# Optimization experiments

Hardware: AMD Instinct MI355X
Metric: run time of the kernel (lower is better)

## Reference

```python
import jax, jax.numpy as jnp
import numpy as np

C = 1000
D = 64
B = 2048
EPS_STATS = 1e-5   # eps in classwise_mean_cov
EPS_PREC = 1e-6    # clamp_min eps in _precision_from_covariance


def setup_inputs() -> dict:
    key = jax.random.key(0)
    kz, ky = jax.random.split(key)
    z = jax.random.normal(kz, (B, D), dtype=jnp.float32)
    y = jax.random.randint(ky, (B,), 0, C, dtype=jnp.int64)
    return {"z": z, "y": y}


def reference(z, y):
    # --- classwise_mean_cov (diag_covariance=True), via segment reductions ---
    # counts per class (+eps), same as one-hot column sums
    ones = jnp.ones((z.shape[0],), dtype=z.dtype)
    class_counts = jax.ops.segment_sum(ones, y, num_segments=C) + EPS_STATS  # (C,)
    class_prior = class_counts / class_counts.sum()                          # (C,)
    class_sums = jax.ops.segment_sum(z, y, num_segments=C)                   # (C,D)
    class_mean = class_sums / class_counts[:, None]                          # (C,D)
    # per-class variance: sum_b [y_b==c] (z_b - mu_c)^2 / counts_c
    centered = z - class_mean[y]                                             # (B,D)
    class_var = jax.ops.segment_sum(centered * centered, y, num_segments=C) / class_counts[:, None]
    pooled_cov = (class_prior[:, None] * class_var).sum(axis=0) + EPS_STATS  # (D,)

    # --- precision (diag): 1 / clamp_min(cov, eps) ---
    precision = 1.0 / jnp.maximum(pooled_cov, EPS_PREC)                      # (D,)

    # --- Mahalanobis scores over all classes ---
    diff = z[:, None, :] - class_mean[None, :, :]                            # (B,C,D)
    m2 = jnp.einsum('bcd,d,bcd->bc', diff, precision, diff)                  # (B,C)
    return jnp.log(class_prior)[None, :] - 0.5 * m2
```

## Files before the change

kernel.cpp:

```cpp
#include <hip/hip_runtime.h>
#include <hip/hip_bf16.h>
#include <math.h>

#define BB 2048
#define CC 1000
#define DD 64
#define NCB 125
#define NTB 16
constexpr float EPS_STATS = 1e-5f;
constexpr float EPS_PREC  = 1e-6f;
constexpr float TSUM = (float)BB + (float)CC * EPS_STATS;

typedef __attribute__((ext_vector_type(8))) short bf8;
typedef __attribute__((ext_vector_type(4))) float f32x4;

__device__ inline unsigned short f2bf(float f) {
    __hip_bfloat16 h = __float2bfloat16(f);
    return *reinterpret_cast<unsigned short*>(&h);
}

__global__ void __launch_bounds__(256)
k_stats(const float* __restrict__ z, const int* __restrict__ y,
        float* __restrict__ mean, float* __restrict__ logpr,
        float* __restrict__ corrPart, float* __restrict__ T2part) {
    int tid = threadIdx.x, bid = blockIdx.x;
    if (bid < NCB) {
        __shared__ __align__(16) int ys[BB];
        __shared__ int mlist[BB];
        __shared__ float sacc[8 * DD];
        __shared__ float corrv[8 * DD];
        __shared__ int cnts[8];
        __shared__ int mcnt;

        const int4* y4 = reinterpret_cast<const int4*>(y);
        int4* ys4 = reinterpret_cast<int4*>(ys);
        ys4[tid] = y4[tid];
        ys4[tid + 256] = y4[tid + 256];
        sacc[tid] = 0.f; sacc[tid + 256] = 0.f;
        if (tid < 8) cnts[tid] = 0;
        if (tid == 0) mcnt = 0;
        __syncthreads();

        int cbase = bid * 8;
        #pragma unroll
        for (int i = 0; i < BB / 256; ++i) {
            int b = tid + i * 256;
            int cl = ys[b] - cbase;
            if ((unsigned)cl < 8u) {
                atomicAdd(&cnts[cl], 1);
                int p = atomicAdd(&mcnt, 1);
                mlist[p] = b * 8 + cl;
            }
        }
        __syncthreads();

        int n = mcnt;
        int w = tid >> 6, lane = tid & 63;
        int eg = w * 4 + (lane >> 4);
        int d4 = (lane & 15) * 4;
        for (int j0 = 0; j0 < n; j0 += 16) {
            int j = j0 + eg;
            if (j < n) {
                int e = mlist[j];
                float4 v = *reinterpret_cast<const float4*>(
                    &z[(size_t)(e >> 3) * DD + d4]);
                float* sa = &sacc[(e & 7) * DD + d4];
                atomicAdd(sa + 0, v.x);
                atomicAdd(sa + 1, v.y);
                atomicAdd(sa + 2, v.z);
                atomicAdd(sa + 3, v.w);
            }
        }
        __syncthreads();

        #pragma unroll
        for (int i = 0; i < 2; ++i) {
            int idx = tid + i * 256;
            int cl = idx >> 6, d = idx & 63;
            float s  = sacc[idx];
            float nn = (float)cnts[cl];
            float ce = nn + EPS_STATS;
            float inv = 1.0f / ce;
            int c = cbase + cl;
            mean[(size_t)c * DD + d] = s * inv;
            if (d == 0) logpr[c] = logf(ce / TSUM);
            corrv[idx] = s * s * (nn + 2.f * EPS_STATS) * inv * inv;
        }
        __syncthreads();
        if (tid < DD) {
            float a = 0.f;
            #pragma unroll
            for (int cl = 0; cl < 8; ++cl) a += corrv[cl * DD + tid];
            corrPart[bid * DD + tid] = a;
        }
    } else {
        __shared__ float p2[4][DD];
        int tb = bid - NCB;
        int d = tid & 63, grp = tid >> 6;
        int r0 = tb * 128 + grp * 32;
        float a = 0.f;
        #pragma unroll 8
        for (int r = 0; r < 32; ++r) {
            float v = z[(size_t)(r0 + r) * DD + d];
            a = fmaf(v, v, a);
        }
        p2[grp][d] = a;
        __syncthreads();
        if (tid < DD)
            T2part[tb * DD + tid] =
                p2[0][tid] + p2[1][tid] + p2[2][tid] + p2[3][tid];
    }
}

__global__ void __launch_bounds__(256)
k_score_mfma(const float* __restrict__ z, const float* __restrict__ mean,
             const float* __restrict__ logpr, const float* __restrict__ corrPart,
             const float* __restrict__ T2part, float* __restrict__ out) {
    __shared__ __align__(16) float red[16][DD];
    __shared__ float ps_s[DD];
    int tid = threadIdx.x;

    {
        int r0 = tid >> 4;
        int c4 = (tid & 15) * 4;
        float4 t = *reinterpret_cast<const float4*>(&T2part[r0 * DD + c4]);
        float ax = t.x, ay = t.y, az = t.z, aw = t.w;
        for (int p = r0; p < NCB; p += 16) {
            float4 v = *reinterpret_cast<const float4*>(&corrPart[p * DD + c4]);
            ax -= v.x; ay -= v.y; az -= v.z; aw -= v.w;
        }
        float4 a4 = {ax, ay, az, aw};
        *reinterpret_cast<float4*>(&red[r0][c4]) = a4;
    }
    __syncthreads();
    if (tid < DD) {
        float acc = 0.f;
        #pragma unroll
        for (int g = 0; g < 16; ++g) acc += red[g][tid];
        float pooled = acc / TSUM + EPS_STATS;
        ps_s[tid] = 1.0f / fmaxf(pooled, EPS_PREC);
    }
    __syncthreads();

    int wv = tid >> 6, l = tid & 63;
    int lr = l & 15, lg = l >> 4;
    int b0 = blockIdx.x * 64 + wv * 16;
    int c0 = blockIdx.y * 64;

    float ps0[8], ps1[8];
    #pragma unroll
    for (int j = 0; j < 8; ++j) { ps0[j] = ps_s[lg * 8 + j]; ps1[j] = ps_s[32 + lg * 8 + j]; }

    const float* zrow = z + (size_t)(b0 + lr) * DD;
    float4 z00 = *reinterpret_cast<const float4*>(zrow + lg * 8);
    float4 z01 = *reinterpret_cast<const float4*>(zrow + lg * 8 + 4);
    float4 z10 = *reinterpret_cast<const float4*>(zrow + 32 + lg * 8);
    float4 z11 = *reinterpret_cast<const float4*>(zrow + 32 + lg * 8 + 4);
    float zf0[8] = {z00.x, z00.y, z00.z, z00.w, z01.x, z01.y, z01.z, z01.w};
    float zf1[8] = {z10.x, z10.y, z10.z, z10.w, z11.x, z11.y, z11.z, z11.w};
    bf8 a0, a1;
    float sbp = 0.f;
    #pragma unroll
    for (int j = 0; j < 8; ++j) {
        a0[j] = (short)f2bf(zf0[j]);
        a1[j] = (short)f2bf(zf1[j]);
        sbp = fmaf(ps0[j] * zf0[j], zf0[j], sbp);
        sbp = fmaf(ps1[j] * zf1[j], zf1[j], sbp);
    }
    sbp += __shfl_xor(sbp, 16);
    sbp += __shfl_xor(sbp, 32);

    f32x4 acc[4];
    float cstv[4];
    #pragma unroll
    for (int ct = 0; ct < 4; ++ct) {
        int c = c0 + ct * 16 + lr;
        int cm = (c < CC) ? c : (CC - 1);
        const float* mrow = mean + (size_t)cm * DD;
        float4 m00 = *reinterpret_cast<const float4*>(mrow + lg * 8);
        float4 m01 = *reinterpret_cast<const float4*>(mrow + lg * 8 + 4);
        float4 m10 = *reinterpret_cast<const float4*>(mrow + 32 + lg * 8);
        float4 m11 = *reinterpret_cast<const float4*>(mrow + 32 + lg * 8 + 4);
        float mf0[8] = {m00.x, m00.y, m00.z, m00.w, m01.x, m01.y, m01.z, m01.w};
        float mf1[8] = {m10.x, m10.y, m10.z, m10.w, m11.x, m11.y, m11.z, m11.w};
        bf8 w0, w1;
        float kc = 0.f;
        #pragma unroll
        for (int j = 0; j < 8; ++j) {
            float wf0 = ps0[j] * mf0[j], wf1 = ps1[j] * mf1[j];
            w0[j] = (short)f2bf(wf0);
            w1[j] = (short)f2bf(wf1);
            kc = fmaf(wf0, mf0[j], kc);
            kc = fmaf(wf1, mf1[j], kc);
        }
        kc += __shfl_xor(kc, 16);
        kc += __shfl_xor(kc, 32);
        cstv[ct] = fmaf(-0.5f, kc, logpr[cm]);
        f32x4 a = {0.f, 0.f, 0.f, 0.f};
        a = __builtin_amdgcn_mfma_f32_16x16x32_bf16(a0, w0, a, 0, 0, 0);
        a = __builtin_amdgcn_mfma_f32_16x16x32_bf16(a1, w1, a, 0, 0, 0);
        acc[ct] = a;
    }

    float sbv[4];
    #pragma unroll
    for (int r = 0; r < 4; ++r) sbv[r] = __shfl(sbp, lg * 4 + r);
    #pragma unroll
    for (int ct = 0; ct < 4; ++ct) {
        int c = c0 + ct * 16 + lr;
        if (c < CC) {
            #pragma unroll
            for (int r = 0; r < 4; ++r) {
                int b = b0 + lg * 4 + r;
                out[(size_t)b * CC + c] = acc[ct][r] + cstv[ct] - 0.5f * sbv[r];
            }
        }
    }
}

extern "C" void kernel_launch(void* const* d_in, const int* in_sizes, int n_in,
                              void* d_out, int out_size, void* d_ws, size_t ws_size,
                              hipStream_t stream) {
    const float* z = (const float*)d_in[0];
    const int*   y = (const int*)d_in[1];
    float* out = (float*)d_out;

    float* mean     = (float*)d_ws;
    float* logpr    = mean + DD * CC;
    float* corrPart = logpr + CC;
    float* T2part   = corrPart + NCB * DD;

    k_stats<<<NCB + NTB, 256, 0, stream>>>(z, y, mean, logpr, corrPart, T2part);
    dim3 grid(BB / 64, (CC + 63) / 64);
    k_score_mfma<<<grid, 256, 0, stream>>>(z, mean, logpr, corrPart, T2part, out);
}
```

Before: 21.05 us.

## Fuse sum-of-squares into classwise stats blocks and double classes per block

```diff
diff --git a/kernel.cpp b/kernel.cpp
--- a/kernel.cpp
+++ b/kernel.cpp
@@ -5,8 +5,8 @@
 #define BB 2048
 #define CC 1000
 #define DD 64
-#define NCB 125
-#define NTB 16
+#define CPB 16
+#define NCB 63
 constexpr float EPS_STATS = 1e-5f;
 constexpr float EPS_PREC  = 1e-6f;
 constexpr float TSUM = (float)BB + (float)CC * EPS_STATS;
@@ -22,100 +22,96 @@
 __global__ void __launch_bounds__(256)
 k_stats(const float* __restrict__ z, const int* __restrict__ y,
         float* __restrict__ mean, float* __restrict__ logpr,
-        float* __restrict__ corrPart, float* __restrict__ T2part) {
+        float* __restrict__ part) {
+    __shared__ __align__(16) int ys[BB];
+    __shared__ int mlist[BB];
+    __shared__ float sacc[CPB * DD];
+    __shared__ float corrv[CPB * DD];
+    __shared__ float t2s[DD];
+    __shared__ int cnts[CPB];
+    __shared__ int mcnt;
     int tid = threadIdx.x, bid = blockIdx.x;
-    if (bid < NCB) {
-        __shared__ __align__(16) int ys[BB];
-        __shared__ int mlist[BB];
-        __shared__ float sacc[8 * DD];
-        __shared__ float corrv[8 * DD];
-        __shared__ int cnts[8];
-        __shared__ int mcnt;
-
-        const int4* y4 = reinterpret_cast<const int4*>(y);
-        int4* ys4 = reinterpret_cast<int4*>(ys);
-        ys4[tid] = y4[tid];
-        ys4[tid + 256] = y4[tid + 256];
-        sacc[tid] = 0.f; sacc[tid + 256] = 0.f;
-        if (tid < 8) cnts[tid] = 0;
-        if (tid == 0) mcnt = 0;
-        __syncthreads();
-
-        int cbase = bid * 8;
-        #pragma unroll
-        for (int i = 0; i < BB / 256; ++i) {
-            int b = tid + i * 256;
-            int cl = ys[b] - cbase;
-            if ((unsigned)cl < 8u) {
-                atomicAdd(&cnts[cl], 1);
-                int p = atomicAdd(&mcnt, 1);
-                mlist[p] = b * 8 + cl;
-            }
-        }
-        __syncthreads();
-
-        int n = mcnt;
-        int w = tid >> 6, lane = tid & 63;
-        int eg = w * 4 + (lane >> 4);
-        int d4 = (lane & 15) * 4;
-        for (int j0 = 0; j0 < n; j0 += 16) {
-            int j = j0 + eg;
-            if (j < n) {
-                int e = mlist[j];
-                float4 v = *reinterpret_cast<const float4*>(
-                    &z[(size_t)(e >> 3) * DD + d4]);
-                float* sa = &sacc[(e & 7) * DD + d4];
-                atomicAdd(sa + 0, v.x);
-                atomicAdd(sa + 1, v.y);
-                atomicAdd(sa + 2, v.z);
-                atomicAdd(sa + 3, v.w);
-            }
-        }
-        __syncthreads();
-
-        #pragma unroll
-        for (int i = 0; i < 2; ++i) {
-            int idx = tid + i * 256;
-            int cl = idx >> 6, d = idx & 63;
-            float s  = sacc[idx];
-            float nn = (float)cnts[cl];
-            float ce = nn + EPS_STATS;
-            float inv = 1.0f / ce;
-            int c = cbase + cl;
+
+    const int4* y4 = reinterpret_cast<const int4*>(y);
+    int4* ys4 = reinterpret_cast<int4*>(ys);
+    ys4[tid] = y4[tid];
+    ys4[tid + 256] = y4[tid + 256];
+    #pragma unroll
+    for (int i = 0; i < CPB * DD / 256; ++i) sacc[tid + i * 256] = 0.f;
+    if (tid < DD) t2s[tid] = 0.f;
+    if (tid < CPB) cnts[tid] = 0;
+    if (tid == 0) mcnt = 0;
+    __syncthreads();
+
+    int cbase = bid * CPB;
+    #pragma unroll
+    for (int i = 0; i < BB / 256; ++i) {
+        int b = tid + i * 256;
+        int cl = ys[b] - cbase;
+        if ((unsigned)cl < (unsigned)CPB) {
+            atomicAdd(&cnts[cl], 1);
+            int p = atomicAdd(&mcnt, 1);
+            mlist[p] = b * CPB + cl;
+        }
+    }
+    __syncthreads();
+
+    int n = mcnt;
+    int w = tid >> 6, lane = tid & 63;
+    int eg = w * 4 + (lane >> 4);
+    int d4 = (lane & 15) * 4;
+    float t2x = 0.f, t2y = 0.f, t2z = 0.f, t2w = 0.f;
+    for (int j0 = 0; j0 < n; j0 += 16) {
+        int j = j0 + eg;
+        if (j < n) {
+            int e = mlist[j];
+            float4 v = *reinterpret_cast<const float4*>(
+                &z[(size_t)(e / CPB) * DD + d4]);
+            float* sa = &sacc[(e % CPB) * DD + d4];
+            atomicAdd(sa + 0, v.x);
+            atomicAdd(sa + 1, v.y);
+            atomicAdd(sa + 2, v.z);
+            atomicAdd(sa + 3, v.w);
+            t2x = fmaf(v.x, v.x, t2x);
+            t2y = fmaf(v.y, v.y, t2y);
+            t2z = fmaf(v.z, v.z, t2z);
+            t2w = fmaf(v.w, v.w, t2w);
+        }
+    }
+    atomicAdd(&t2s[d4 + 0], t2x);
+    atomicAdd(&t2s[d4 + 1], t2y);
+    atomicAdd(&t2s[d4 + 2], t2z);
+    atomicAdd(&t2s[d4 + 3], t2w);
+    __syncthreads();
+
+    #pragma unroll
+    for (int i = 0; i < CPB * DD / 256; ++i) {
+        int idx = tid + i * 256;
+        int cl = idx >> 6, d = idx & 63;
+        float s  = sacc[idx];
+        float nn = (float)cnts[cl];
+        float ce = nn + EPS_STATS;
+        float inv = 1.0f / ce;
+        int c = cbase + cl;
+        if (c < CC) {
             mean[(size_t)c * DD + d] = s * inv;
             if (d == 0) logpr[c] = logf(ce / TSUM);
-            corrv[idx] = s * s * (nn + 2.f * EPS_STATS) * inv * inv;
-        }
-        __syncthreads();
-        if (tid < DD) {
-            float a = 0.f;
-            #pragma unroll
-            for (int cl = 0; cl < 8; ++cl) a += corrv[cl * DD + tid];
-            corrPart[bid * DD + tid] = a;
-        }
-    } else {
-        __shared__ float p2[4][DD];
-        int tb = bid - NCB;
-        int d = tid & 63, grp = tid >> 6;
-        int r0 = tb * 128 + grp * 32;
-        float a = 0.f;
-        #pragma unroll 8
-        for (int r = 0; r < 32; ++r) {
-            float v = z[(size_t)(r0 + r) * DD + d];
-            a = fmaf(v, v, a);
-        }
-        p2[grp][d] = a;
-        __syncthreads();
-        if (tid < DD)
-            T2part[tb * DD + tid] =
-                p2[0][tid] + p2[1][tid] + p2[2][tid] + p2[3][tid];
+        }
+        corrv[idx] = s * s * (nn + 2.f * EPS_STATS) * inv * inv;
+    }
+    __syncthreads();
+    if (tid < DD) {
+        float a = t2s[tid];
+        #pragma unroll
+        for (int cl = 0; cl < CPB; ++cl) a -= corrv[cl * DD + tid];
+        part[bid * DD + tid] = a;
     }
 }
 
 __global__ void __launch_bounds__(256)
 k_score_mfma(const float* __restrict__ z, const float* __restrict__ mean,
-             const float* __restrict__ logpr, const float* __restrict__ corrPart,
-             const float* __restrict__ T2part, float* __restrict__ out) {
+             const float* __restrict__ logpr, const float* __restrict__ part,
+             float* __restrict__ out) {
     __shared__ __align__(16) float red[16][DD];
     __shared__ float ps_s[DD];
     int tid = threadIdx.x;
@@ -123,11 +119,10 @@
     {
         int r0 = tid >> 4;
         int c4 = (tid & 15) * 4;
-        float4 t = *reinterpret_cast<const float4*>(&T2part[r0 * DD + c4]);
-        float ax = t.x, ay = t.y, az = t.z, aw = t.w;
+        float ax = 0.f, ay = 0.f, az = 0.f, aw = 0.f;
         for (int p = r0; p < NCB; p += 16) {
-            float4 v = *reinterpret_cast<const float4*>(&corrPart[p * DD + c4]);
-            ax -= v.x; ay -= v.y; az -= v.z; aw -= v.w;
+            float4 v = *reinterpret_cast<const float4*>(&part[p * DD + c4]);
+            ax += v.x; ay += v.y; az += v.z; aw += v.w;
         }
         float4 a4 = {ax, ay, az, aw};
         *reinterpret_cast<float4*>(&red[r0][c4]) = a4;
@@ -225,12 +220,11 @@
     const int*   y = (const int*)d_in[1];
     float* out = (float*)d_out;
 
-    float* mean     = (float*)d_ws;
-    float* logpr    = mean + DD * CC;
-    float* corrPart = logpr + CC;
-    float* T2part   = corrPart + NCB * DD;
-
-    k_stats<<<NCB + NTB, 256, 0, stream>>>(z, y, mean, logpr, corrPart, T2part);
+    float* mean  = (float*)d_ws;
+    float* logpr = mean + DD * CC;
+    float* part  = logpr + CC;
+
+    k_stats<<<NCB, 256, 0, stream>>>(z, y, mean, logpr, part);
     dim3 grid(BB / 64, (CC + 63) / 64);
-    k_score_mfma<<<grid, 256, 0, stream>>>(z, mean, logpr, corrPart, T2part, out);
-}
+    k_score_mfma<<<grid, 256, 0, stream>>>(z, mean, logpr, part, out);
+}
```

New measurement: 22.95 us. 1.09x slower.
